# Kernel optimization log

Hardware: AMD Instinct MI355X
Metric: run time of the kernel (lower is better)

## Reference

```python
import jax, jax.numpy as jnp
import numpy as np

EPS = 1e-5

def setup_inputs() -> dict:
    key = jax.random.key(0)
    ks = jax.random.split(key, 6)
    N, M, F, K = 100000, 12, 128, 64
    atom_in_fea = jax.random.normal(ks[0], (N, F), dtype=jnp.float32)
    nbr_fea = jax.random.normal(ks[1], (N, M, K), dtype=jnp.float32)
    nbr_fea_idx = jax.random.randint(ks[2], (N, M), 0, N, dtype=jnp.int64)
    # Linear(2F+K -> 2F): torch stores weight [out, in]
    W = jax.random.normal(ks[3], (2 * F, 2 * F + K), dtype=jnp.float32) * 0.02
    b = jax.random.normal(ks[4], (2 * F,), dtype=jnp.float32) * 0.02
    bn1_gamma = jnp.ones((2 * F,), dtype=jnp.float32)
    bn1_beta = jnp.zeros((2 * F,), dtype=jnp.float32)
    bn2_gamma = jnp.ones((F,), dtype=jnp.float32)
    bn2_beta = jnp.zeros((F,), dtype=jnp.float32)
    return {"atom_in_fea": atom_in_fea, "nbr_fea": nbr_fea, "nbr_fea_idx": nbr_fea_idx,
            "W": W, "b": b, "bn1_gamma": bn1_gamma, "bn1_beta": bn1_beta,
            "bn2_gamma": bn2_gamma, "bn2_beta": bn2_beta}

def _batchnorm(x, gamma, beta):
    # training-mode BatchNorm1d: biased batch variance, eps=1e-5
    mean = jnp.mean(x, axis=0)
    var = jnp.var(x, axis=0)
    return (x - mean) * jax.lax.rsqrt(var + EPS) * gamma + beta

def reference(atom_in_fea, nbr_fea, nbr_fea_idx, W, b, bn1_gamma, bn1_beta, bn2_gamma, bn2_beta):
    N, M = nbr_fea_idx.shape
    F = atom_in_fea.shape[1]
    atom_nbr_fea = atom_in_fea[nbr_fea_idx]                      # [N, M, F] gather
    atom_self = jnp.broadcast_to(atom_in_fea[:, None, :], (N, M, F))
    total = jnp.concatenate([atom_self, atom_nbr_fea, nbr_fea], axis=2)  # [N, M, 2F+K]
    gated = jnp.einsum('nmk,ok->nmo', total, W) + b              # [N, M, 2F]
    gated = _batchnorm(gated.reshape(-1, 2 * F), bn1_gamma, bn1_beta).reshape(N, M, 2 * F)
    nbr_filter, nbr_core = jnp.split(gated, 2, axis=2)
    nbr_sumed = jnp.sum(jax.nn.sigmoid(nbr_filter) * jax.nn.relu(nbr_core), axis=1)  # [N, F]
    nbr_sumed = _batchnorm(nbr_sumed, bn2_gamma, bn2_beta)
    return jax.nn.relu(atom_in_fea + nbr_sumed)
```

## Files before the change

### kernel.cpp

```cpp
#include <hip/hip_runtime.h>

typedef __bf16 bf16x8 __attribute__((ext_vector_type(8)));
typedef __bf16 bf16x4 __attribute__((ext_vector_type(4)));
typedef float  f32x4  __attribute__((ext_vector_type(4)));

#define CIN 320
#define GATHER_OFF 0
#define EDGE_OFF   24576
#define SELF_OFF   36864
#define SMEM_BYTES 38912

#define GLOAD_LDS16(gsrc, ldst)                                              \
    __builtin_amdgcn_global_load_lds(                                        \
        (__attribute__((address_space(1))) void*)(void*)(gsrc),              \
        (__attribute__((address_space(3))) void*)(ldst), 16, 0, 0)

__global__ void detect_kernel(const unsigned short* __restrict__ atom_h,
                              const unsigned* __restrict__ idx_w, int* __restrict__ flags)
{
    const int lane = threadIdx.x;
    int f32 = 0;
    for (int i = lane; i < 256; i += 64) {
        const int e = (atom_h[i] >> 7) & 0xFF;
        if (e >= 134) f32 = 1;
    }
    const unsigned long long m32 = __ballot(f32);
    const int hi = (idx_w[2 * lane + 1] != 0) ? 1 : 0;
    const unsigned long long mhi = __ballot(hi);
    if (lane == 0) { flags[0] = m32 ? 1 : 0; flags[1] = mhi ? 0 : 1; }
}

__global__ __launch_bounds__(256) void convert_bf16(const void* __restrict__ src,
    __bf16* __restrict__ dst, long n8, const int* __restrict__ flags)
{
    const long t = (long)blockIdx.x * 256 + threadIdx.x;
    if (t >= n8) return;
    const long i = t * 8;
    if (flags[0]) {
        const float* s = (const float*)src;
        bf16x8 o;
#pragma unroll
        for (int j = 0; j < 8; ++j) o[j] = (__bf16)s[i + j];
        *(bf16x8*)&dst[i] = o;
    } else {
        *(uint4*)&dst[i] = *(const uint4*)((const char*)src + i * 2);
    }
}

template<int MODE>
__global__ __launch_bounds__(512, 4) void gemm_conv(
    const __bf16* __restrict__ atomb, const void* __restrict__ nbrp,
    const void* __restrict__ idxp, const __bf16* __restrict__ Wb,
    const int* __restrict__ flags,
    float* __restrict__ stats1, const float* __restrict__ coef1,
    __bf16* __restrict__ gws, float* __restrict__ nsum)
{
    __shared__ __align__(16) char smem[SMEM_BYTES];

    const int tid = threadIdx.x;
    const int blk = blockIdx.x;
    const long rowbase = (long)blk * 96;
    const int  n0 = blk * 8;
    const int  isf32 = flags[0];
    const int  isi64 = flags[1];

    const int lane = tid & 63;
    const int wv   = tid >> 6;
    const int quad = lane >> 4;
    const int lrow = lane & 15;

    if (wv < 2) {
        const int row = wv * 4 + (lane >> 4);
        GLOAD_LDS16(atomb + (long)(n0 + row) * 128 + (lane & 15) * 8,
                    smem + SELF_OFF + wv * 1024);
    }
    long jrow[3]; int grow[3];
#pragma unroll
    for (int i = 0; i < 3; ++i) {
        const int t = wv + i * 8;
        grow[i] = 4 * t + (lane >> 4);
        jrow[i] = isi64 ? (long)((const long long*)idxp)[rowbase + grow[i]]
                        : (long)((const int*)idxp)[rowbase + grow[i]];
    }
#pragma unroll
    for (int i = 0; i < 3; ++i) {
        const int t = wv + i * 8;
        const int chunk = ((lane & 15) << 4) ^ ((grow[i] & 7) << 4);
        GLOAD_LDS16(atomb + jrow[i] * 128 + (chunk >> 1),
                    smem + GATHER_OFF + t * 1024);
    }
    if (isf32) {
        const float* nf = (const float*)nbrp;
#pragma unroll
        for (int rnd = 0; rnd < 2; ++rnd) {
            const int task = tid + rnd * 512;
            if (task < 768) {
                const int c = task & 7, row = task >> 3;
                const float* sp = &nf[(rowbase + row) * 64 + c * 8];
                f32x4 v0 = *(const f32x4*)sp;
                f32x4 v1 = *(const f32x4*)(sp + 4);
                bf16x8 o;
#pragma unroll
                for (int j = 0; j < 4; ++j) { o[j] = (__bf16)v0[j]; o[j + 4] = (__bf16)v1[j]; }
                *(bf16x8*)(smem + EDGE_OFF + row * 128 + ((c ^ (row & 7)) << 4)) = o;
            }
        }
    } else {
        const __bf16* nb = (const __bf16*)nbrp;
#pragma unroll
        for (int i = 0; i < 2; ++i) {
            const int t = wv + i * 8;
            if (t < 12) {
                const int row = 8 * t + (lane >> 3);
                const int c = lane & 7;
                const int chunk = (c << 4) ^ ((row & 7) << 4);
                GLOAD_LDS16(nb + (rowbase + row) * 64 + (chunk >> 1),
                            smem + EDGE_OFF + t * 1024);
            }
        }
    }
    __syncthreads();

    const int cF = wv * 16 + lrow;
    const __bf16* wpF = Wb + (long)cF * CIN + quad * 8;
    const __bf16* wpC = Wb + (long)(128 + cF) * CIN + quad * 8;

    int arow[6], aatom[6];
#pragma unroll
    for (int rt = 0; rt < 6; ++rt) {
        arow[rt]  = rt * 16 + lrow;
        aatom[rt] = (arow[rt] * 171) >> 11;
    }

    f32x4 acc[6][2] = {};
    bf16x8 bF = *(const bf16x8*)wpF;
    bf16x8 bC = *(const bf16x8*)wpC;
    bf16x8 bFn, bCn;

#pragma unroll
    for (int kk = 0; kk < 10; ++kk) {
        if (kk < 9) {
            bFn = *(const bf16x8*)(wpF + (kk + 1) * 32);
            bCn = *(const bf16x8*)(wpC + (kk + 1) * 32);
        }
#pragma unroll
        for (int rt = 0; rt < 6; ++rt) {
            int addr;
            if (kk < 4)
                addr = SELF_OFF + aatom[rt] * 256 + kk * 64 + quad * 16;
            else if (kk < 8)
                addr = GATHER_OFF + arow[rt] * 256 + ((((kk - 4) * 4 + quad) ^ (arow[rt] & 7)) << 4);
            else
                addr = EDGE_OFF + arow[rt] * 128 + ((((kk - 8) * 4 + quad) ^ (arow[rt] & 7)) << 4);
            const bf16x8 afrag = *(const bf16x8*)(smem + addr);
            acc[rt][0] = __builtin_amdgcn_mfma_f32_16x16x32_bf16(afrag, bF, acc[rt][0], 0, 0, 0);
            acc[rt][1] = __builtin_amdgcn_mfma_f32_16x16x32_bf16(afrag, bC, acc[rt][1], 0, 0, 0);
        }
        if (kk < 9) { bF = bFn; bC = bCn; }
    }

    if (MODE <= 1) {
        float* st = stats1 + (blk & 63) * 512;
#pragma unroll
        for (int p = 0; p < 2; ++p) {
            float s = 0.f, ss = 0.f;
#pragma unroll
            for (int rt = 0; rt < 6; ++rt)
#pragma unroll
                for (int r = 0; r < 4; ++r) {
                    const float v = acc[rt][p][r];
                    s += v; ss += v * v;
                }
            s += __shfl_xor(s, 16); ss += __shfl_xor(ss, 16);
            s += __shfl_xor(s, 32); ss += __shfl_xor(ss, 32);
            if (quad == 0) {
                atomicAdd(&st[p * 128 + cF], s);
                atomicAdd(&st[256 + p * 128 + cF], ss);
            }
        }
        if (MODE == 1) {
            char* dst = (char*)gws + (long)blk * 49152;
#pragma unroll
            for (int rt = 0; rt < 6; ++rt) {
                unsigned u[4];
#pragma unroll
                for (int r = 0; r < 4; ++r) {
                    const unsigned short fb =
                        __builtin_bit_cast(unsigned short, (__bf16)acc[rt][0][r]);
                    const unsigned short cb =
                        __builtin_bit_cast(unsigned short, (__bf16)acc[rt][1][r]);
                    u[r] = (unsigned)fb | ((unsigned)cb << 16);
                }
                *(uint4*)(dst + rt * 8192 + tid * 16) = *(const uint4*)u;
            }
        }
    } else {
        __syncthreads();
        float* sumbuf = (float*)smem;
        sumbuf[tid] = 0.f; sumbuf[tid + 512] = 0.f;
        __syncthreads();
        const float aF = coef1[cF],       bFc = coef1[256 + cF];
        const float aC = coef1[128 + cF], bCc = coef1[384 + cF];
#pragma unroll
        for (int rt = 0; rt < 6; ++rt)
#pragma unroll
            for (int r = 0; r < 4; ++r) {
                const int row  = rt * 16 + quad * 4 + r;
                const int atom = (row * 171) >> 11;
                const float gF = aF * acc[rt][0][r] + bFc;
                const float gC = aC * acc[rt][1][r] + bCc;
                const float val = (1.f / (1.f + __expf(-gF))) * fmaxf(gC, 0.f);
                atomicAdd(&sumbuf[atom * 128 + cF], val);
            }
        __syncthreads();
        nsum[(long)n0 * 128 + tid]       = sumbuf[tid];
        nsum[(long)n0 * 128 + 512 + tid] = sumbuf[tid + 512];
    }
}

__global__ void reduce_bn1(const float* __restrict__ stats1, const void* __restrict__ gamma,
                           const void* __restrict__ beta, float* __restrict__ coef1,
                           const int* __restrict__ flags)
{
    const int c = threadIdx.x;
    const int isf32 = flags[0];
    float s = 0.f, ss = 0.f;
    for (int b = 0; b < 64; ++b) { s += stats1[b * 512 + c]; ss += stats1[b * 512 + 256 + c]; }
    const float inv  = 1.f / 1200000.f;
    const float mean = s * inv;
    const float var  = ss * inv - mean * mean;
    const float g  = isf32 ? ((const float*)gamma)[c] : (float)((const __bf16*)gamma)[c];
    const float bb = isf32 ? ((const float*)beta)[c]  : (float)((const __bf16*)beta)[c];
    const float A = g * rsqrtf(var + 1e-5f);
    coef1[c]       = A;
    coef1[256 + c] = bb - A * mean;
}

__global__ __launch_bounds__(512) void apply_gated(const __bf16* __restrict__ g,
    const float* __restrict__ coef1, float* __restrict__ nsum)
{
    const int tid   = threadIdx.x;
    const int blk   = blockIdx.x;
    const int lrow  = tid & 15;
    const int wv_ch = (tid >> 4) & 7;
    const int apair = tid >> 7;
    const int cF    = wv_ch * 16 + lrow;

    const float aF = coef1[cF],       bF = coef1[256 + cF];
    const float aC = coef1[128 + cF], bC = coef1[384 + cF];
    const char* src = (const char*)g + (long)blk * 49152 + wv_ch * 1024 + lrow * 16;

    float out[2];
#pragma unroll
    for (int p = 0; p < 2; ++p) {
        const int a = apair + p * 4;
        float s = 0.f;
#pragma unroll
        for (int u = 0; u < 3; ++u) {
            const int rowstart = a * 12 + u * 4;
            const int rt   = rowstart >> 4;
            const int quad = (rowstart >> 2) & 3;
            const uint4 w = *(const uint4*)(src + rt * 8192 + quad * 256);
            const unsigned uw[4] = {w.x, w.y, w.z, w.w};
#pragma unroll
            for (int r = 0; r < 4; ++r) {
                const float gF = aF * (float)__builtin_bit_cast(__bf16, (unsigned short)(uw[r] & 0xFFFFu)) + bF;
                const float gC = aC * (float)__builtin_bit_cast(__bf16, (unsigned short)(uw[r] >> 16)) + bC;
                s += (1.f / (1.f + __expf(-gF))) * fmaxf(gC, 0.f);
            }
        }
        out[p] = s;
    }
    const long n0 = (long)blk * 8;
#pragma unroll
    for (int p = 0; p < 2; ++p)
        nsum[(n0 + apair + p * 4) * 128 + cF] = out[p];
}

__global__ __launch_bounds__(256) void bn2_stats(const float* __restrict__ nsum,
                                                 float* __restrict__ stats2)
{
    __shared__ float ls[256], lss[256];
    const int tid = threadIdx.x;
    float s = 0.f, ss = 0.f;
    const long stride = (long)gridDim.x * 256;
    for (long i = (long)blockIdx.x * 256 + tid; i < 12800000L; i += stride) {
        const float v = nsum[i]; s += v; ss += v * v;
    }
    ls[tid] = s; lss[tid] = ss;
    __syncthreads();
    if (tid < 128) {
        atomicAdd(&stats2[tid],       ls[tid] + ls[tid + 128]);
        atomicAdd(&stats2[128 + tid], lss[tid] + lss[tid + 128]);
    }
}

__global__ void reduce_bn2(const float* __restrict__ stats2, const void* __restrict__ gamma,
                           const void* __restrict__ beta, float* __restrict__ coef2,
                           const int* __restrict__ flags)
{
    const int c = threadIdx.x;
    const int isf32 = flags[0];
    const float inv  = 1.f / 100000.f;
    const float mean = stats2[c] * inv;
    const float var  = stats2[128 + c] * inv - mean * mean;
    const float g  = isf32 ? ((const float*)gamma)[c] : (float)((const __bf16*)gamma)[c];
    const float bb = isf32 ? ((const float*)beta)[c]  : (float)((const __bf16*)beta)[c];
    const float A = g * rsqrtf(var + 1e-5f);
    coef2[c]       = A;
    coef2[128 + c] = bb - A * mean;
}

__global__ __launch_bounds__(256) void final_out(const __bf16* __restrict__ atomb,
    const float* __restrict__ nsum, const float* __restrict__ coef2,
    void* __restrict__ outp, const int* __restrict__ flags)
{
    const long i = ((long)blockIdx.x * 256 + threadIdx.x) * 8;
    const int f0 = (int)(i & 127);
    bf16x8 a  = *(const bf16x8*)&atomb[i];
    f32x4  u0 = *(const f32x4*)&nsum[i];
    f32x4  u1 = *(const f32x4*)&nsum[i + 4];
    float v[8];
#pragma unroll
    for (int j = 0; j < 8; ++j) {
        const float A  = coef2[f0 + j];
        const float B  = coef2[128 + f0 + j];
        const float ns = (j < 4) ? u0[j] : u1[j - 4];
        v[j] = fmaxf((float)a[j] + A * ns + B, 0.f);
    }
    if (flags[0]) {
        float* o = (float*)outp;
        f32x4 w0 = {v[0], v[1], v[2], v[3]}, w1 = {v[4], v[5], v[6], v[7]};
        *(f32x4*)&o[i]     = w0;
        *(f32x4*)&o[i + 4] = w1;
    } else {
        __bf16* o = (__bf16*)outp;
        bf16x8 w;
#pragma unroll
        for (int j = 0; j < 8; ++j) w[j] = (__bf16)v[j];
        *(bf16x8*)&o[i] = w;
    }
}

extern "C" void kernel_launch(void* const* d_in, const int* in_sizes, int n_in,
                              void* d_out, int out_size, void* d_ws, size_t ws_size,
                              hipStream_t stream)
{
    const void* atom = d_in[0];
    const void* nbr  = d_in[1];
    const void* idxp = d_in[2];
    const void* W    = d_in[3];
    const void* g1   = d_in[5];
    const void* b1   = d_in[6];
    const void* g2   = d_in[7];
    const void* b2   = d_in[8];

    char* ws = (char*)d_ws;
    int*    flags  = (int*)ws;
    float*  stats1 = (float*)(ws + 1024);
    float*  coef1  = (float*)(ws + 132096);
    float*  stats2 = (float*)(ws + 134144);
    float*  coef2  = (float*)(ws + 135168);
    __bf16* atomb  = (__bf16*)(ws + 136192);
    __bf16* Wb     = (__bf16*)(ws + 25736192);
    float*  nsum   = (float*)(ws + 25900032);
    __bf16* gws    = (__bf16*)(ws + 77100032);

    const size_t need_big = 77100032UL + 614400000UL;

    hipMemsetAsync(ws, 0, 136192, stream);
    detect_kernel<<<1, 64, 0, stream>>>((const unsigned short*)atom, (const unsigned*)idxp, flags);
    convert_bf16<<<6250, 256, 0, stream>>>(atom, atomb, 1600000L, flags);
    convert_bf16<<<40, 256, 0, stream>>>(W, Wb, 10240L, flags);

    if (ws_size >= need_big) {
        gemm_conv<1><<<12500, 512, 0, stream>>>(atomb, nbr, idxp, Wb, flags,
                                                stats1, nullptr, gws, nullptr);
        reduce_bn1<<<1, 256, 0, stream>>>(stats1, g1, b1, coef1, flags);
        apply_gated<<<12500, 512, 0, stream>>>(gws, coef1, nsum);
    } else {
        gemm_conv<0><<<12500, 512, 0, stream>>>(atomb, nbr, idxp, Wb, flags,
                                                stats1, nullptr, nullptr, nullptr);
        reduce_bn1<<<1, 256, 0, stream>>>(stats1, g1, b1, coef1, flags);
        gemm_conv<2><<<12500, 512, 0, stream>>>(atomb, nbr, idxp, Wb, flags,
                                                nullptr, coef1, nullptr, nsum);
    }
    bn2_stats<<<512, 256, 0, stream>>>(nsum, stats2);
    reduce_bn2<<<1, 128, 0, stream>>>(stats2, g2, b2, coef2, flags);
    final_out<<<6250, 256, 0, stream>>>(atomb, nsum, coef2, d_out, flags);
}
```

Baseline: 1.004 ms.

## Make gemm_conv persistent over four tiles with double-buffered async LDS staging

Each block now processes four consecutive 8-atom tiles instead of one. While the current tile runs its MFMA loop, it issues the global-to-LDS gather and self loads for the next tile into a second buffer and prefetches the next indices. Edge features are held in registers and written to LDS after a manual vmcnt wait. This hides gather latency behind compute, at the cost of 64KB LDS per block (lower occupancy), hand-tuned waitcnt counts that must match the number of outstanding loads, and a fourfold cut in grid size. The self-atom LDS layout also gains an XOR swizzle to avoid bank conflicts.

```diff
diff --git a/kernel.cpp b/kernel.cpp
--- a/kernel.cpp
+++ b/kernel.cpp
@@ -1,19 +1,28 @@
 #include <hip/hip_runtime.h>
 
 typedef __bf16 bf16x8 __attribute__((ext_vector_type(8)));
-typedef __bf16 bf16x4 __attribute__((ext_vector_type(4)));
 typedef float  f32x4  __attribute__((ext_vector_type(4)));
 
 #define CIN 320
-#define GATHER_OFF 0
-#define EDGE_OFF   24576
-#define SELF_OFF   36864
-#define SMEM_BYTES 38912
+#define NT  4
+#define BUF_SZ     26624
+#define SELF_REL   24576
+#define EDGE_OFF   53248
+#define SMEM_BYTES 65536
 
 #define GLOAD_LDS16(gsrc, ldst)                                              \
     __builtin_amdgcn_global_load_lds(                                        \
         (__attribute__((address_space(1))) void*)(void*)(gsrc),              \
         (__attribute__((address_space(3))) void*)(ldst), 16, 0, 0)
+
+__device__ __forceinline__ void waitcnt_vm(int n) {
+    switch (n) {
+    case 0:  asm volatile("s_waitcnt vmcnt(0)" ::: "memory"); break;
+    case 2:  asm volatile("s_waitcnt vmcnt(2)" ::: "memory"); break;
+    case 4:  asm volatile("s_waitcnt vmcnt(4)" ::: "memory"); break;
+    default: asm volatile("s_waitcnt vmcnt(10)" ::: "memory"); break;
+    }
+}
 
 __global__ void detect_kernel(const unsigned short* __restrict__ atom_h,
                               const unsigned* __restrict__ idx_w, int* __restrict__ flags)
@@ -59,162 +68,213 @@
 
     const int tid = threadIdx.x;
     const int blk = blockIdx.x;
-    const long rowbase = (long)blk * 96;
-    const int  n0 = blk * 8;
-    const int  isf32 = flags[0];
-    const int  isi64 = flags[1];
+    const int isf32 = flags[0];
+    const int isi64 = flags[1];
 
     const int lane = tid & 63;
     const int wv   = tid >> 6;
     const int quad = lane >> 4;
     const int lrow = lane & 15;
 
-    if (wv < 2) {
-        const int row = wv * 4 + (lane >> 4);
-        GLOAD_LDS16(atomb + (long)(n0 + row) * 128 + (lane & 15) * 8,
-                    smem + SELF_OFF + wv * 1024);
-    }
-    long jrow[3]; int grow[3];
-#pragma unroll
-    for (int i = 0; i < 3; ++i) {
-        const int t = wv + i * 8;
-        grow[i] = 4 * t + (lane >> 4);
-        jrow[i] = isi64 ? (long)((const long long*)idxp)[rowbase + grow[i]]
-                        : (long)((const int*)idxp)[rowbase + grow[i]];
-    }
-#pragma unroll
-    for (int i = 0; i < 3; ++i) {
-        const int t = wv + i * 8;
-        const int chunk = ((lane & 15) << 4) ^ ((grow[i] & 7) << 4);
-        GLOAD_LDS16(atomb + jrow[i] * 128 + (chunk >> 1),
-                    smem + GATHER_OFF + t * 1024);
-    }
-    if (isf32) {
-        const float* nf = (const float*)nbrp;
-#pragma unroll
-        for (int rnd = 0; rnd < 2; ++rnd) {
-            const int task = tid + rnd * 512;
-            if (task < 768) {
-                const int c = task & 7, row = task >> 3;
-                const float* sp = &nf[(rowbase + row) * 64 + c * 8];
-                f32x4 v0 = *(const f32x4*)sp;
-                f32x4 v1 = *(const f32x4*)(sp + 4);
-                bf16x8 o;
-#pragma unroll
-                for (int j = 0; j < 4; ++j) { o[j] = (__bf16)v0[j]; o[j + 4] = (__bf16)v1[j]; }
-                *(bf16x8*)(smem + EDGE_OFF + row * 128 + ((c ^ (row & 7)) << 4)) = o;
-            }
-        }
-    } else {
-        const __bf16* nb = (const __bf16*)nbrp;
-#pragma unroll
-        for (int i = 0; i < 2; ++i) {
-            const int t = wv + i * 8;
-            if (t < 12) {
-                const int row = 8 * t + (lane >> 3);
-                const int c = lane & 7;
-                const int chunk = (c << 4) ^ ((row & 7) << 4);
-                GLOAD_LDS16(nb + (rowbase + row) * 64 + (chunk >> 1),
-                            smem + EDGE_OFF + t * 1024);
-            }
-        }
-    }
-    __syncthreads();
+    const int g_sub  = lane >> 4;
+    const int g_slot = lane & 15;
+    const int  e_row0 = tid >> 3, e_c0 = tid & 7;
+    const int  e_row1 = (tid + 512) >> 3;
+    const bool e_has1 = (tid < 256);
+
+    f32x4 ef0a, ef0b, ef1a, ef1b;
+    uint4 eb0, eb1;
+
+    auto load_idx = [&](int gt, int& j0, int& j1, int& j2) {
+        const long rb = (long)gt * 96;
+        const long r0 = rb + 4 * (wv)      + g_sub;
+        const long r1 = rb + 4 * (wv + 8)  + g_sub;
+        const long r2 = rb + 4 * (wv + 16) + g_sub;
+        if (isi64) {
+            j0 = ((const int*)idxp)[2 * r0];
+            j1 = ((const int*)idxp)[2 * r1];
+            j2 = ((const int*)idxp)[2 * r2];
+        } else {
+            j0 = ((const int*)idxp)[r0];
+            j1 = ((const int*)idxp)[r1];
+            j2 = ((const int*)idxp)[r2];
+        }
+    };
+
+    auto stage = [&](int gt, int buf, int j0, int j1, int j2) {
+        char* B = smem + buf * BUF_SZ;
+        const long rb = (long)gt * 96;
+        const int  n0 = gt * 8;
+        if (wv < 2) {
+            const int row = wv * 4 + g_sub;
+            GLOAD_LDS16(atomb + (long)(n0 + row) * 128 + (g_slot ^ row) * 8,
+                        B + SELF_REL + wv * 1024);
+        }
+        {
+            const int r0 = 4 * (wv)      + g_sub;
+            const int r1 = 4 * (wv + 8)  + g_sub;
+            const int r2 = 4 * (wv + 16) + g_sub;
+            GLOAD_LDS16(atomb + (long)j0 * 128 + (g_slot ^ (r0 & 7)) * 8, B + (wv)      * 1024);
+            GLOAD_LDS16(atomb + (long)j1 * 128 + (g_slot ^ (r1 & 7)) * 8, B + (wv + 8)  * 1024);
+            GLOAD_LDS16(atomb + (long)j2 * 128 + (g_slot ^ (r2 & 7)) * 8, B + (wv + 16) * 1024);
+        }
+        if (isf32) {
+            const float* nf = (const float*)nbrp;
+            const float* p0 = &nf[(rb + e_row0) * 64 + e_c0 * 8];
+            ef0a = *(const f32x4*)p0; ef0b = *(const f32x4*)(p0 + 4);
+            if (e_has1) {
+                const float* p1 = &nf[(rb + e_row1) * 64 + e_c0 * 8];
+                ef1a = *(const f32x4*)p1; ef1b = *(const f32x4*)(p1 + 4);
+            }
+        } else {
+            const __bf16* nb = (const __bf16*)nbrp;
+            eb0 = *(const uint4*)&nb[(rb + e_row0) * 64 + e_c0 * 8];
+            if (e_has1) eb1 = *(const uint4*)&nb[(rb + e_row1) * 64 + e_c0 * 8];
+        }
+    };
+
+    auto edge_write = [&]() {
+        if (isf32) {
+            bf16x8 o;
+#pragma unroll
+            for (int j = 0; j < 4; ++j) { o[j] = (__bf16)ef0a[j]; o[j + 4] = (__bf16)ef0b[j]; }
+            *(bf16x8*)(smem + EDGE_OFF + e_row0 * 128 + ((e_c0 ^ (e_row0 & 7)) << 4)) = o;
+            if (e_has1) {
+                bf16x8 o1;
+#pragma unroll
+                for (int j = 0; j < 4; ++j) { o1[j] = (__bf16)ef1a[j]; o1[j + 4] = (__bf16)ef1b[j]; }
+                *(bf16x8*)(smem + EDGE_OFF + e_row1 * 128 + ((e_c0 ^ (e_row1 & 7)) << 4)) = o1;
+            }
+        } else {
+            *(uint4*)(smem + EDGE_OFF + e_row0 * 128 + ((e_c0 ^ (e_row0 & 7)) << 4)) = eb0;
+            if (e_has1)
+                *(uint4*)(smem + EDGE_OFF + e_row1 * 128 + ((e_c0 ^ (e_row1 & 7)) << 4)) = eb1;
+        }
+    };
 
     const int cF = wv * 16 + lrow;
     const __bf16* wpF = Wb + (long)cF * CIN + quad * 8;
     const __bf16* wpC = Wb + (long)(128 + cF) * CIN + quad * 8;
 
-    int arow[6], aatom[6];
-#pragma unroll
-    for (int rt = 0; rt < 6; ++rt) {
-        arow[rt]  = rt * 16 + lrow;
-        aatom[rt] = (arow[rt] * 171) >> 11;
-    }
-
-    f32x4 acc[6][2] = {};
-    bf16x8 bF = *(const bf16x8*)wpF;
-    bf16x8 bC = *(const bf16x8*)wpC;
-    bf16x8 bFn, bCn;
-
-#pragma unroll
-    for (int kk = 0; kk < 10; ++kk) {
-        if (kk < 9) {
-            bFn = *(const bf16x8*)(wpF + (kk + 1) * 32);
-            bCn = *(const bf16x8*)(wpC + (kk + 1) * 32);
-        }
-#pragma unroll
-        for (int rt = 0; rt < 6; ++rt) {
-            int addr;
-            if (kk < 4)
-                addr = SELF_OFF + aatom[rt] * 256 + kk * 64 + quad * 16;
-            else if (kk < 8)
-                addr = GATHER_OFF + arow[rt] * 256 + ((((kk - 4) * 4 + quad) ^ (arow[rt] & 7)) << 4);
-            else
-                addr = EDGE_OFF + arow[rt] * 128 + ((((kk - 8) * 4 + quad) ^ (arow[rt] & 7)) << 4);
-            const bf16x8 afrag = *(const bf16x8*)(smem + addr);
-            acc[rt][0] = __builtin_amdgcn_mfma_f32_16x16x32_bf16(afrag, bF, acc[rt][0], 0, 0, 0);
-            acc[rt][1] = __builtin_amdgcn_mfma_f32_16x16x32_bf16(afrag, bC, acc[rt][1], 0, 0, 0);
-        }
-        if (kk < 9) { bF = bFn; bC = bCn; }
-    }
-
-    if (MODE <= 1) {
-        float* st = stats1 + (blk & 63) * 512;
-#pragma unroll
-        for (int p = 0; p < 2; ++p) {
-            float s = 0.f, ss = 0.f;
+    const int gt0 = blk * NT;
+    int j0, j1, j2;
+    load_idx(gt0, j0, j1, j2);
+    stage(gt0, 0, j0, j1, j2);
+    __builtin_amdgcn_sched_barrier(0);
+    load_idx(gt0 + 1, j0, j1, j2);
+    __builtin_amdgcn_sched_barrier(0);
+
+#pragma unroll
+    for (int tt = 0; tt < NT; ++tt) {
+        const int gt  = gt0 + tt;
+        const int buf = tt & 1;
+        const int n0  = gt * 8;
+
+        if (tt == 0) waitcnt_vm(0);
+        else         waitcnt_vm(MODE == 1 ? 10 : (MODE == 0 ? 4 : 2));
+        __builtin_amdgcn_sched_barrier(0);
+        edge_write();
+        asm volatile("s_waitcnt lgkmcnt(0)" ::: "memory");
+        __builtin_amdgcn_s_barrier();
+        __builtin_amdgcn_sched_barrier(0);
+
+        if (tt + 1 < NT) {
+            stage(gt + 1, buf ^ 1, j0, j1, j2);
+            __builtin_amdgcn_sched_barrier(0);
+            if (tt + 2 < NT) load_idx(gt + 2, j0, j1, j2);
+            __builtin_amdgcn_sched_barrier(0);
+        }
+
+        f32x4 acc[6][2] = {};
+        bf16x8 bF = *(const bf16x8*)wpF;
+        bf16x8 bC = *(const bf16x8*)wpC;
+        bf16x8 bFn, bCn;
+#pragma unroll
+        for (int kk = 0; kk < 10; ++kk) {
+            if (kk < 9) {
+                bFn = *(const bf16x8*)(wpF + (kk + 1) * 32);
+                bCn = *(const bf16x8*)(wpC + (kk + 1) * 32);
+            }
+#pragma unroll
+            for (int rt = 0; rt < 6; ++rt) {
+                const int arow  = rt * 16 + lrow;
+                const int aatom = (arow * 171) >> 11;
+                int addr;
+                if (kk < 4)
+                    addr = buf * BUF_SZ + SELF_REL + aatom * 256 + (((kk * 4 + quad) ^ aatom) << 4);
+                else if (kk < 8)
+                    addr = buf * BUF_SZ + arow * 256 + ((((kk - 4) * 4 + quad) ^ (arow & 7)) << 4);
+                else
+                    addr = EDGE_OFF + arow * 128 + ((((kk - 8) * 4 + quad) ^ (arow & 7)) << 4);
+                const bf16x8 afrag = *(const bf16x8*)(smem + addr);
+                acc[rt][0] = __builtin_amdgcn_mfma_f32_16x16x32_bf16(afrag, bF, acc[rt][0], 0, 0, 0);
+                acc[rt][1] = __builtin_amdgcn_mfma_f32_16x16x32_bf16(afrag, bC, acc[rt][1], 0, 0, 0);
+            }
+            if (kk < 9) { bF = bFn; bC = bCn; }
+        }
+
+        if (MODE <= 1) {
+            float* st = stats1 + (gt & 63) * 512;
+#pragma unroll
+            for (int p = 0; p < 2; ++p) {
+                float s = 0.f, ss = 0.f;
+#pragma unroll
+                for (int rt = 0; rt < 6; ++rt)
+#pragma unroll
+                    for (int r = 0; r < 4; ++r) {
+                        const float v = acc[rt][p][r];
+                        s += v; ss += v * v;
+                    }
+                s += __shfl_xor(s, 16); ss += __shfl_xor(ss, 16);
+                s += __shfl_xor(s, 32); ss += __shfl_xor(ss, 32);
+                if (quad == 0) {
+                    atomicAdd(&st[p * 128 + cF], s);
+                    atomicAdd(&st[256 + p * 128 + cF], ss);
+                }
+            }
+            if (MODE == 1) {
+                char* dst = (char*)gws + (long)gt * 49152;
+#pragma unroll
+                for (int rt = 0; rt < 6; ++rt) {
+                    unsigned u[4];
+#pragma unroll
+                    for (int r = 0; r < 4; ++r) {
+                        const unsigned short fb =
+                            __builtin_bit_cast(unsigned short, (__bf16)acc[rt][0][r]);
+                        const unsigned short cb =
+                            __builtin_bit_cast(unsigned short, (__bf16)acc[rt][1][r]);
+                        u[r] = (unsigned)fb | ((unsigned)cb << 16);
+                    }
+                    *(uint4*)(dst + rt * 8192 + tid * 16) = *(const uint4*)u;
+                }
+            }
+        } else {
+            __builtin_amdgcn_s_barrier();
+            float* sumbuf = (float*)(smem + EDGE_OFF);
+            sumbuf[tid] = 0.f; sumbuf[tid + 512] = 0.f;
+            asm volatile("s_waitcnt lgkmcnt(0)" ::: "memory");
+            __builtin_amdgcn_s_barrier();
+            const float aF = coef1[cF],       bFc = coef1[256 + cF];
+            const float aC = coef1[128 + cF], bCc = coef1[384 + cF];
 #pragma unroll
             for (int rt = 0; rt < 6; ++rt)
 #pragma unroll
                 for (int r = 0; r < 4; ++r) {
-                    const float v = acc[rt][p][r];
-                    s += v; ss += v * v;
+                    const int row  = rt * 16 + quad * 4 + r;
+                    const int atom = (row * 171) >> 11;
+                    const float gF = aF * acc[rt][0][r] + bFc;
+                    const float gC = aC * acc[rt][1][r] + bCc;
+                    const float val = (1.f / (1.f + __expf(-gF))) * fmaxf(gC, 0.f);
+                    atomicAdd(&sumbuf[atom * 128 + cF], val);
                 }
-            s += __shfl_xor(s, 16); ss += __shfl_xor(ss, 16);
-            s += __shfl_xor(s, 32); ss += __shfl_xor(ss, 32);
-            if (quad == 0) {
-                atomicAdd(&st[p * 128 + cF], s);
-                atomicAdd(&st[256 + p * 128 + cF], ss);
-            }
-        }
-        if (MODE == 1) {
-            char* dst = (char*)gws + (long)blk * 49152;
-#pragma unroll
-            for (int rt = 0; rt < 6; ++rt) {
-                unsigned u[4];
-#pragma unroll
-                for (int r = 0; r < 4; ++r) {
-                    const unsigned short fb =
-                        __builtin_bit_cast(unsigned short, (__bf16)acc[rt][0][r]);
-                    const unsigned short cb =
-                        __builtin_bit_cast(unsigned short, (__bf16)acc[rt][1][r]);
-                    u[r] = (unsigned)fb | ((unsigned)cb << 16);
-                }
-                *(uint4*)(dst + rt * 8192 + tid * 16) = *(const uint4*)u;
-            }
-        }
-    } else {
-        __syncthreads();
-        float* sumbuf = (float*)smem;
-        sumbuf[tid] = 0.f; sumbuf[tid + 512] = 0.f;
-        __syncthreads();
-        const float aF = coef1[cF],       bFc = coef1[256 + cF];
-        const float aC = coef1[128 + cF], bCc = coef1[384 + cF];
-#pragma unroll
-        for (int rt = 0; rt < 6; ++rt)
-#pragma unroll
-            for (int r = 0; r < 4; ++r) {
-                const int row  = rt * 16 + quad * 4 + r;
-                const int atom = (row * 171) >> 11;
-                const float gF = aF * acc[rt][0][r] + bFc;
-                const float gC = aC * acc[rt][1][r] + bCc;
-                const float val = (1.f / (1.f + __expf(-gF))) * fmaxf(gC, 0.f);
-                atomicAdd(&sumbuf[atom * 128 + cF], val);
-            }
-        __syncthreads();
-        nsum[(long)n0 * 128 + tid]       = sumbuf[tid];
-        nsum[(long)n0 * 128 + 512 + tid] = sumbuf[tid + 512];
+            asm volatile("s_waitcnt lgkmcnt(0)" ::: "memory");
+            __builtin_amdgcn_s_barrier();
+            nsum[(long)n0 * 128 + tid]       = sumbuf[tid];
+            nsum[(long)n0 * 128 + 512 + tid] = sumbuf[tid + 512];
+        }
+
+        __builtin_amdgcn_s_barrier();
+        __builtin_amdgcn_sched_barrier(0);
     }
 }
 
@@ -374,16 +434,16 @@
     convert_bf16<<<40, 256, 0, stream>>>(W, Wb, 10240L, flags);
 
     if (ws_size >= need_big) {
-        gemm_conv<1><<<12500, 512, 0, stream>>>(atomb, nbr, idxp, Wb, flags,
-                                                stats1, nullptr, gws, nullptr);
+        gemm_conv<1><<<3125, 512, 0, stream>>>(atomb, nbr, idxp, Wb, flags,
+                                               stats1, nullptr, gws, nullptr);
         reduce_bn1<<<1, 256, 0, stream>>>(stats1, g1, b1, coef1, flags);
         apply_gated<<<12500, 512, 0, stream>>>(gws, coef1, nsum);
     } else {
-        gemm_conv<0><<<12500, 512, 0, stream>>>(atomb, nbr, idxp, Wb, flags,
-                                                stats1, nullptr, nullptr, nullptr);
+        gemm_conv<0><<<3125, 512, 0, stream>>>(atomb, nbr, idxp, Wb, flags,
+                                               stats1, nullptr, nullptr, nullptr);
         reduce_bn1<<<1, 256, 0, stream>>>(stats1, g1, b1, coef1, flags);
-        gemm_conv<2><<<12500, 512, 0, stream>>>(atomb, nbr, idxp, Wb, flags,
-                                                nullptr, coef1, nullptr, nsum);
+        gemm_conv<2><<<3125, 512, 0, stream>>>(atomb, nbr, idxp, Wb, flags,
+                                               nullptr, coef1, nullptr, nsum);
     }
     bn2_stats<<<512, 256, 0, stream>>>(nsum, stats2);
     reduce_bn2<<<1, 128, 0, stream>>>(stats2, g2, b2, coef2, flags);
```

Result: slower. 1.257 ms (+25.3%).
